# Kernel optimization log

Hardware: AMD Instinct MI355X
Metric: run time of the kernel (lower is better)

## Reference

```python
import jax, jax.numpy as jnp
import numpy as np

B, H, S, DK = 4, 16, 4096, 64


def setup_inputs() -> dict:
    key = jax.random.key(0)
    kq, kk, kv = jax.random.split(key, 3)
    Q = jax.random.normal(kq, (B, H, S, DK), dtype=jnp.float32)
    K = jax.random.normal(kk, (B, H, S, DK), dtype=jnp.float32)
    V = jax.random.normal(kv, (B, H, S, DK), dtype=jnp.float32)
    return {"Q": Q, "K": K, "V": V}


def reference(Q, K, V):
    d_k = K.shape[-1]
    inv_sqrt_dk = jnp.sqrt(jnp.float32(1.0) / d_k)
    # [B, H, S, S] materialized scores (faithful to the naive original)
    scores = jnp.einsum('bhqd,bhkd->bhqk', Q, K) * inv_sqrt_dk
    # causal mask: original subtracts (1 - tril) * 1e9 from scores
    s_q, s_k = Q.shape[-2], K.shape[-2]
    causal = jnp.tril(jnp.ones((s_q, s_k), dtype=jnp.float32))
    scores = scores - (1.0 - causal) * 1e9
    probs = jax.nn.softmax(scores, axis=-1)
    out = jnp.einsum('bhqk,bhkd->bhqd', probs, V)
    return out
```

## Files before the change

### kernel.cpp

```cpp
#include <hip/hip_runtime.h>
#include <hip/hip_bf16.h>

typedef short bf16x8 __attribute__((ext_vector_type(8)));
typedef float f32x16 __attribute__((ext_vector_type(16)));
typedef float f32x4v __attribute__((ext_vector_type(4)));

static constexpr int SEQ = 4096;
static constexpr int HD  = 64;
static constexpr int BQ  = 128;
static constexpr float QSCALE = 0.125f * 1.44269504088896340736f;

union F8 { bf16x8 v; unsigned short u[8]; uint4 q; };

__device__ __forceinline__ unsigned short f2bf(float x) {
    __bf16 b = (__bf16)x;
    return __builtin_bit_cast(unsigned short, b);
}
__device__ __forceinline__ unsigned pk2(float lo, float hi) {
    return (unsigned)f2bf(lo) | ((unsigned)f2bf(hi) << 16);
}
__device__ __forceinline__ float exp2fast(float x) {
    return __builtin_amdgcn_exp2f(x);
}

__device__ __forceinline__ int kperm_src(int rho) {
    return (rho & 0x23) | (((rho >> 3) & 1) << 4) |
           (((rho >> 2) & 1) << 3) | (((rho >> 4) & 1) << 2);
}
__device__ __forceinline__ int kperm_dst(int src) {
    return (src & 0x23) | (((src >> 2) & 1) << 4) |
           (((src >> 4) & 1) << 3) | (((src >> 3) & 1) << 2);
}

__global__ __launch_bounds__(256)
void prep_kv(const float* __restrict__ K, const float* __restrict__ V,
             unsigned short* __restrict__ ws)
{
    __shared__ float vt[64][68];

    const int tid = threadIdx.x;
    const int bid = blockIdx.x;
    const size_t sbase = ((size_t)(bid >> 6)) * (SEQ * HD) +
                         ((size_t)(bid & 63)) * (64 * HD);
    unsigned short* Kt = ws + (size_t)bid * 4096;
    unsigned short* Vt = ws + (size_t)16777216 + (size_t)bid * 4096;

    #pragma unroll
    for (int i = 0; i < 2; ++i) {
        const int c   = tid + 256 * i;
        const int row = c >> 3, j = c & 7;
        const int jsrc = j ^ (row & 7);
        const float* src = K + sbase + kperm_src(row) * HD + 8 * jsrc;
        float4 a = *(const float4*)src;
        float4 b = *(const float4*)(src + 4);
        *(uint4*)(Kt + row * 64 + 8 * j) =
            make_uint4(pk2(a.x, a.y), pk2(a.z, a.w), pk2(b.x, b.y), pk2(b.z, b.w));
    }

    {
        const int r  = tid >> 2;
        const int cb = (tid & 3) << 4;
        const float* src = V + sbase + r * HD + cb;
        *(float4*)&vt[r][cb + 0]  = *(const float4*)(src);
        *(float4*)&vt[r][cb + 4]  = *(const float4*)(src + 4);
        *(float4*)&vt[r][cb + 8]  = *(const float4*)(src + 8);
        *(float4*)&vt[r][cb + 12] = *(const float4*)(src + 12);
    }
    __syncthreads();
    #pragma unroll
    for (int i = 0; i < 2; ++i) {
        const int c = tid + 256 * i;
        const int d = c >> 3, j = c & 7;
        const int kb = 8 * (j ^ (d & 7));
        unsigned u[4];
        #pragma unroll
        for (int p = 0; p < 4; ++p)
            u[p] = pk2(vt[kb + 2 * p][d], vt[kb + 2 * p + 1][d]);
        *(uint4*)(Vt + d * 64 + 8 * j) = make_uint4(u[0], u[1], u[2], u[3]);
    }
}

__global__ __launch_bounds__(256, 2)
void mha_fwd2(const float* __restrict__ Q, float* __restrict__ O,
              const unsigned short* __restrict__ ws)
{
    __shared__ __align__(16) unsigned short LDSu[32768];

    const int tid  = threadIdx.x;
    const int lane = tid & 63;
    const int w    = tid >> 6;
    const int l31  = lane & 31;
    const int h    = lane >> 5;

    const int bid = blockIdx.x;
    const int bh  = bid & 63;
    const int qb  = 31 - (bid >> 6);
    const int q0  = qb * BQ;
    const size_t base = (size_t)bh * (SEQ * HD);

    const int qlane = q0 + 32 * w + l31;

    bf16x8 qf[4];
    {
        const float* qrow = Q + base + (size_t)qlane * HD;
        #pragma unroll
        for (int c = 0; c < 4; ++c) {
            const f32x4v x = *(const f32x4v*)(qrow + 16 * c + 8 * h);
            const f32x4v y = *(const f32x4v*)(qrow + 16 * c + 8 * h + 4);
            F8 f;
            #pragma unroll
            for (int j = 0; j < 4; ++j) f.u[j]     = f2bf(x[j] * QSCALE);
            #pragma unroll
            for (int j = 0; j < 4; ++j) f.u[4 + j] = f2bf(y[j] * QSCALE);
            qf[c] = f.v;
        }
    }

    F8 onesf;
    #pragma unroll
    for (int j = 0; j < 8; ++j) onesf.u[j] = 0x3F80;

    f32x16 oacc[2];
    f32x16 lacc;
    f32x16 zacc;
    #pragma unroll
    for (int r = 0; r < 16; ++r) {
        oacc[0][r] = 0.f; oacc[1][r] = 0.f; lacc[r] = 0.f; zacc[r] = 0.f;
    }

    const int nkt2 = qb + 1;

    char* lds0 = (char*)&LDSu[0];
    const int sw = (l31 & 7) << 4;
    char* a4[4];
    #pragma unroll
    for (int c = 0; c < 4; ++c)
        a4[c] = lds0 + l31 * 128 + (((c << 5) | (h << 4)) ^ sw);

    const unsigned short* Kws = ws;
    const unsigned short* Vws = ws + (size_t)16777216;

    auto stage = [&](int buf, int kt2) {
        const size_t toff = (((size_t)bh << 6) + ((size_t)kt2 << 1)) << 12;
        const int bufoff = buf << 14;
        #pragma unroll
        for (int i = 0; i < 4; ++i) {
            const int ch = 4 * w + i;
            const unsigned short* kg = Kws + toff + ch * 512 + lane * 8;
            const unsigned short* vg = Vws + toff + ch * 512 + lane * 8;
            __builtin_amdgcn_global_load_lds(
                (const __attribute__((address_space(1))) void*)(const void*)kg,
                (__attribute__((address_space(3))) void*)(void*)(lds0 + bufoff + ch * 1024),
                16, 0, 0);
            __builtin_amdgcn_global_load_lds(
                (const __attribute__((address_space(1))) void*)(const void*)vg,
                (__attribute__((address_space(3))) void*)(void*)(lds0 + 32768 + bufoff + ch * 1024),
                16, 0, 0);
        }
    };

    stage(0, 0);
    __syncthreads();

    for (int kt2 = 0; kt2 < nkt2; ++kt2) {
        const bool hn = (kt2 + 1) < nkt2;
        if (hn) stage((kt2 & 1) ^ 1, kt2 + 1);

        const int k0 = kt2 * 128;

        f32x16 sacc[4];
        #pragma unroll
        for (int s = 0; s < 4; ++s) {
            const int t = s >> 1, u = s & 1;
            __builtin_amdgcn_s_setprio(1);
            #pragma unroll
            for (int c = 0; c < 4; ++c) {
                bf16x8 kf = *(const bf16x8*)(a4[c] + t * 8192 + u * 4096);
                sacc[s] = __builtin_amdgcn_mfma_f32_32x32x16_bf16(
                    kf, qf[c], c == 0 ? zacc : sacc[s], 0, 0, 0);
            }
            __builtin_amdgcn_s_setprio(0);
        }

        if (kt2 == nkt2 - 1) {
            #pragma unroll
            for (int s = 0; s < 4; ++s)
                #pragma unroll
                for (int r = 0; r < 16; ++r) {
                    const int key = k0 + 64 * (s >> 1) + 32 * (s & 1) +
                                    16 * ((r >> 2) & 1) + 4 * ((r >> 3) & 1) +
                                    8 * h + (r & 3);
                    if (key > qlane) sacc[s][r] = -1e30f;
                }
        }

        #pragma unroll
        for (int kc = 0; kc < 8; ++kc) {
            const int s = kc >> 1, m0 = kc & 1;
            const int t = kc >> 2, kcl = kc & 3;
            float e0 = exp2fast(sacc[s][4 * m0 + 0]);
            float e1 = exp2fast(sacc[s][4 * m0 + 1]);
            float e2 = exp2fast(sacc[s][4 * m0 + 2]);
            float e3 = exp2fast(sacc[s][4 * m0 + 3]);
            float e4 = exp2fast(sacc[s][8 + 4 * m0 + 0]);
            float e5 = exp2fast(sacc[s][8 + 4 * m0 + 1]);
            float e6 = exp2fast(sacc[s][8 + 4 * m0 + 2]);
            float e7 = exp2fast(sacc[s][8 + 4 * m0 + 3]);
            F8 pf;
            pf.q.x = pk2(e0, e1);
            pf.q.y = pk2(e2, e3);
            pf.q.z = pk2(e4, e5);
            pf.q.w = pk2(e6, e7);
            __builtin_amdgcn_s_setprio(1);
            lacc = __builtin_amdgcn_mfma_f32_32x32x16_bf16(onesf.v, pf.v, lacc, 0, 0, 0);
            {
                bf16x8 vf0 = *(const bf16x8*)(a4[kcl] + 32768 + t * 8192 + 0 * 4096);
                oacc[0] = __builtin_amdgcn_mfma_f32_32x32x16_bf16(vf0, pf.v, oacc[0], 0, 0, 0);
                bf16x8 vf1 = *(const bf16x8*)(a4[kcl] + 32768 + t * 8192 + 1 * 4096);
                oacc[1] = __builtin_amdgcn_mfma_f32_32x32x16_bf16(vf1, pf.v, oacc[1], 0, 0, 0);
            }
            __builtin_amdgcn_s_setprio(0);
        }

        #pragma unroll
        for (int c = 0; c < 4; ++c)
            a4[c] = (char*)((size_t)a4[c] ^ 16384);

        __syncthreads();
    }

    const float il = 1.0f / lacc[0];
    float* orow = O + base + (size_t)qlane * HD;
    #pragma unroll
    for (int dsi = 0; dsi < 2; ++dsi)
        #pragma unroll
        for (int g = 0; g < 4; ++g) {
            f32x4v o4;
            #pragma unroll
            for (int j = 0; j < 4; ++j) o4[j] = oacc[dsi][4 * g + j] * il;
            *(f32x4v*)(orow + 32 * dsi + 8 * g + 4 * h) = o4;
        }
}

__global__ __launch_bounds__(256, 4)
void mha_fwd_fb(const float* __restrict__ Q, const float* __restrict__ K,
                const float* __restrict__ V, float* __restrict__ O)
{
    __shared__ unsigned short Kl[2][4096];
    __shared__ unsigned short Vl[2][4096];

    const int tid  = threadIdx.x;
    const int lane = tid & 63;
    const int w    = tid >> 6;
    const int l31  = lane & 31;
    const int h    = lane >> 5;

    const int bid = blockIdx.x;
    const int bh  = bid & 63;
    const int qb  = 31 - (bid >> 6);
    const int q0  = qb * BQ;
    const size_t base = (size_t)bh * (SEQ * HD);

    const int qlane  = q0 + 32 * w + l31;
    const int qmax_w = q0 + 32 * w + 31;

    bf16x8 qf[4];
    {
        const float* qrow = Q + base + (size_t)qlane * HD;
        #pragma unroll
        for (int c = 0; c < 4; ++c) {
            const f32x4v x = *(const f32x4v*)(qrow + 16 * c + 8 * h);
            const f32x4v y = *(const f32x4v*)(qrow + 16 * c + 8 * h + 4);
            F8 f;
            #pragma unroll
            for (int j = 0; j < 4; ++j) f.u[j]     = f2bf(x[j] * QSCALE);
            #pragma unroll
            for (int j = 0; j < 4; ++j) f.u[4 + j] = f2bf(y[j] * QSCALE);
            qf[c] = f.v;
        }
    }

    F8 onesf;
    #pragma unroll
    for (int j = 0; j < 8; ++j) onesf.u[j] = 0x3F80;

    f32x16 oacc[2], lacc, zacc;
    #pragma unroll
    for (int r = 0; r < 16; ++r) {
        oacc[0][r] = 0.f; oacc[1][r] = 0.f; lacc[r] = 0.f; zacc[r] = 0.f;
    }

    const int nkt = 2 * qb + 2;

    const int ksr = tid >> 2;
    const int ksc = (tid & 3) << 4;
    const int vkb = tid >> 4;
    const int vdb = tid & 15;

    f32x4v kreg[4], vreg[4];

    auto load_regs = [&](int kt) {
        const int k0 = kt * 64;
        const float* ks = K + base + (size_t)(k0 + ksr) * HD + ksc;
        kreg[0] = *(const f32x4v*)(ks);
        kreg[1] = *(const f32x4v*)(ks + 4);
        kreg[2] = *(const f32x4v*)(ks + 8);
        kreg[3] = *(const f32x4v*)(ks + 12);
        const float* vs = V + base + (size_t)(k0 + 4 * vkb) * HD + 4 * vdb;
        vreg[0] = *(const f32x4v*)(vs);
        vreg[1] = *(const f32x4v*)(vs + HD);
        vreg[2] = *(const f32x4v*)(vs + 2 * HD);
        vreg[3] = *(const f32x4v*)(vs + 3 * HD);
    };

    auto write_lds = [&](int buf) {
        unsigned u[8];
        #pragma unroll
        for (int i = 0; i < 4; ++i) {
            u[2*i]   = pk2(kreg[i][0], kreg[i][1]);
            u[2*i+1] = pk2(kreg[i][2], kreg[i][3]);
        }
        const int drow = kperm_dst(ksr);
        char* kd = (char*)&Kl[buf][0] + drow * 128;
        const int o0 = (2 * ksc) ^ ((drow & 7) << 4);
        *(uint4*)(kd + o0)        = make_uint4(u[0], u[1], u[2], u[3]);
        *(uint4*)(kd + (o0 ^ 16)) = make_uint4(u[4], u[5], u[6], u[7]);
        #pragma unroll
        for (int i = 0; i < 4; ++i) {
            const int c = (i + (vdb >> 1)) & 3;
            const int d = 4 * vdb + c;
            const unsigned lo = pk2(vreg[0][c], vreg[1][c]);
            const unsigned hi = pk2(vreg[2][c], vreg[3][c]);
            char* vd = (char*)&Vl[buf][0] + d * 128 + ((8 * vkb) ^ ((d & 7) << 4));
            *(uint2*)vd = make_uint2(lo, hi);
        }
    };

    load_regs(0); write_lds(0);
    __syncthreads();

    for (int kt = 0; kt < nkt; ++kt) {
        const int cur = kt & 1;
        const bool hn = (kt + 1) < nkt;
        if (hn) load_regs(kt + 1);

        if (64 * kt <= qmax_w) {
            const unsigned short* Kb = &Kl[cur][0];
            const unsigned short* Vb = &Vl[cur][0];
            const int k0 = kt * 64;

            f32x16 sacc[2];
            #pragma unroll
            for (int s = 0; s < 2; ++s) {
                const int row = 32 * s + l31;
                const char* rp = (const char*)Kb + row * 128;
                const int swl = (row & 7) << 4;
                #pragma unroll
                for (int c = 0; c < 4; ++c) {
                    bf16x8 kf = *(const bf16x8*)(rp + ((32 * c + 16 * h) ^ swl));
                    sacc[s] = __builtin_amdgcn_mfma_f32_32x32x16_bf16(
                        kf, qf[c], c == 0 ? zacc : sacc[s], 0, 0, 0);
                }
            }

            if (kt >= nkt - 2) {
                #pragma unroll
                for (int s = 0; s < 2; ++s)
                    #pragma unroll
                    for (int r = 0; r < 16; ++r) {
                        const int key = k0 + 32 * s + 16 * ((r >> 2) & 1) +
                                        4 * ((r >> 3) & 1) + 8 * h + (r & 3);
                        if (key > qlane) sacc[s][r] = -1e30f;
                    }
            }

            #pragma unroll
            for (int s = 0; s < 2; ++s) {
                #pragma unroll
                for (int r = 0; r < 16; ++r) sacc[s][r] = exp2fast(sacc[s][r]);
                #pragma unroll
                for (int m0 = 0; m0 < 2; ++m0) {
                    const int kc = 2 * s + m0;
                    F8 pf;
                    pf.q.x = pk2(sacc[s][4 * m0 + 0],  sacc[s][4 * m0 + 1]);
                    pf.q.y = pk2(sacc[s][4 * m0 + 2],  sacc[s][4 * m0 + 3]);
                    pf.q.z = pk2(sacc[s][8 + 4 * m0 + 0], sacc[s][8 + 4 * m0 + 1]);
                    pf.q.w = pk2(sacc[s][8 + 4 * m0 + 2], sacc[s][8 + 4 * m0 + 3]);
                    lacc = __builtin_amdgcn_mfma_f32_32x32x16_bf16(onesf.v, pf.v, lacc, 0, 0, 0);
                    #pragma unroll
                    for (int dsi = 0; dsi < 2; ++dsi) {
                        const int row = 32 * dsi + l31;
                        const char* vp = (const char*)Vb + row * 128 +
                                         ((32 * kc + 16 * h) ^ ((row & 7) << 4));
                        bf16x8 vf = *(const bf16x8*)vp;
                        oacc[dsi] = __builtin_amdgcn_mfma_f32_32x32x16_bf16(vf, pf.v, oacc[dsi], 0, 0, 0);
                    }
                }
            }
        }

        if (hn) write_lds(cur ^ 1);
        __syncthreads();
    }

    const float il = 1.0f / lacc[0];
    float* orow = O + base + (size_t)qlane * HD;
    #pragma unroll
    for (int dsi = 0; dsi < 2; ++dsi)
        #pragma unroll
        for (int g = 0; g < 4; ++g) {
            f32x4v o4;
            #pragma unroll
            for (int j = 0; j < 4; ++j) o4[j] = oacc[dsi][4 * g + j] * il;
            *(f32x4v*)(orow + 32 * dsi + 8 * g + 4 * h) = o4;
        }
}

extern "C" void kernel_launch(void* const* d_in, const int* in_sizes, int n_in,
                              void* d_out, int out_size, void* d_ws, size_t ws_size,
                              hipStream_t stream) {
    const float* Q = (const float*)d_in[0];
    const float* K = (const float*)d_in[1];
    const float* V = (const float*)d_in[2];
    float* O = (float*)d_out;
    (void)in_sizes; (void)n_in; (void)out_size;

    const size_t need = (size_t)2 * 16777216 * sizeof(unsigned short);
    if (ws_size >= need) {
        unsigned short* ws = (unsigned short*)d_ws;
        prep_kv<<<dim3(64 * 64), 256, 0, stream>>>(K, V, ws);
        mha_fwd2<<<dim3(32 * 64), 256, 0, stream>>>(Q, O, ws);
    } else {
        mha_fwd_fb<<<dim3(32 * 64), 256, 0, stream>>>(Q, K, V, O);
    }
}
```

Measured before the change: 255.5 us.

## Shrink KV tile to 64 keys with per-wave causal tile skipping

The attention kernel now steps through keys in 64-key tiles instead of 128, which halves LDS use so launch bounds rise to 4 blocks per CU. Each wave skips the compute for tiles that lie entirely above its own causal diagonal, and masking is applied only on the last two tiles. The aims are higher occupancy and less wasted work on masked keys, at the cost of twice as many loop iterations and block-wide barriers per KV range and possible register pressure at the higher occupancy target.

```diff
diff --git a/kernel.cpp b/kernel.cpp
--- a/kernel.cpp
+++ b/kernel.cpp
@@ -80,11 +80,11 @@
     }
 }
 
-__global__ __launch_bounds__(256, 2)
-void mha_fwd2(const float* __restrict__ Q, float* __restrict__ O,
-              const unsigned short* __restrict__ ws)
+__global__ __launch_bounds__(256, 4)
+void mha_fwd(const float* __restrict__ Q, float* __restrict__ O,
+             const unsigned short* __restrict__ ws)
 {
-    __shared__ __align__(16) unsigned short LDSu[32768];
+    __shared__ __align__(16) unsigned short LDSu[16384];
 
     const int tid  = threadIdx.x;
     const int lane = tid & 63;
@@ -98,7 +98,8 @@
     const int q0  = qb * BQ;
     const size_t base = (size_t)bh * (SEQ * HD);
 
-    const int qlane = q0 + 32 * w + l31;
+    const int qlane  = q0 + 32 * w + l31;
+    const int qmax_w = q0 + 32 * w + 31;
 
     bf16x8 qf[4];
     {
@@ -128,7 +129,7 @@
         oacc[0][r] = 0.f; oacc[1][r] = 0.f; lacc[r] = 0.f; zacc[r] = 0.f;
     }
 
-    const int nkt2 = qb + 1;
+    const int nkt = 2 * qb + 2;
 
     char* lds0 = (char*)&LDSu[0];
     const int sw = (l31 & 7) << 4;
@@ -140,12 +141,12 @@
     const unsigned short* Kws = ws;
     const unsigned short* Vws = ws + (size_t)16777216;
 
-    auto stage = [&](int buf, int kt2) {
-        const size_t toff = (((size_t)bh << 6) + ((size_t)kt2 << 1)) << 12;
-        const int bufoff = buf << 14;
-        #pragma unroll
-        for (int i = 0; i < 4; ++i) {
-            const int ch = 4 * w + i;
+    auto stage = [&](int buf, int kt) {
+        const size_t toff = (((size_t)bh << 6) + (size_t)kt) << 12;
+        const int bufoff = buf << 13;
+        #pragma unroll
+        for (int i = 0; i < 2; ++i) {
+            const int ch = 2 * w + i;
             const unsigned short* kg = Kws + toff + ch * 512 + lane * 8;
             const unsigned short* vg = Vws + toff + ch * 512 + lane * 8;
             __builtin_amdgcn_global_load_lds(
@@ -154,7 +155,7 @@
                 16, 0, 0);
             __builtin_amdgcn_global_load_lds(
                 (const __attribute__((address_space(1))) void*)(const void*)vg,
-                (__attribute__((address_space(3))) void*)(void*)(lds0 + 32768 + bufoff + ch * 1024),
+                (__attribute__((address_space(3))) void*)(void*)(lds0 + 16384 + bufoff + ch * 1024),
                 16, 0, 0);
         }
     };
@@ -162,69 +163,68 @@
     stage(0, 0);
     __syncthreads();
 
-    for (int kt2 = 0; kt2 < nkt2; ++kt2) {
-        const bool hn = (kt2 + 1) < nkt2;
-        if (hn) stage((kt2 & 1) ^ 1, kt2 + 1);
-
-        const int k0 = kt2 * 128;
-
-        f32x16 sacc[4];
-        #pragma unroll
-        for (int s = 0; s < 4; ++s) {
-            const int t = s >> 1, u = s & 1;
-            __builtin_amdgcn_s_setprio(1);
-            #pragma unroll
-            for (int c = 0; c < 4; ++c) {
-                bf16x8 kf = *(const bf16x8*)(a4[c] + t * 8192 + u * 4096);
-                sacc[s] = __builtin_amdgcn_mfma_f32_32x32x16_bf16(
-                    kf, qf[c], c == 0 ? zacc : sacc[s], 0, 0, 0);
-            }
-            __builtin_amdgcn_s_setprio(0);
-        }
-
-        if (kt2 == nkt2 - 1) {
-            #pragma unroll
-            for (int s = 0; s < 4; ++s)
-                #pragma unroll
-                for (int r = 0; r < 16; ++r) {
-                    const int key = k0 + 64 * (s >> 1) + 32 * (s & 1) +
-                                    16 * ((r >> 2) & 1) + 4 * ((r >> 3) & 1) +
-                                    8 * h + (r & 3);
-                    if (key > qlane) sacc[s][r] = -1e30f;
+    for (int kt = 0; kt < nkt; ++kt) {
+        const bool hn = (kt + 1) < nkt;
+        if (hn) stage((kt & 1) ^ 1, kt + 1);
+
+        if (64 * kt <= qmax_w) {
+            const int k0 = kt * 64;
+
+            f32x16 sacc[2];
+            #pragma unroll
+            for (int s = 0; s < 2; ++s) {
+                __builtin_amdgcn_s_setprio(1);
+                #pragma unroll
+                for (int c = 0; c < 4; ++c) {
+                    bf16x8 kf = *(const bf16x8*)(a4[c] + s * 4096);
+                    sacc[s] = __builtin_amdgcn_mfma_f32_32x32x16_bf16(
+                        kf, qf[c], c == 0 ? zacc : sacc[s], 0, 0, 0);
                 }
-        }
-
-        #pragma unroll
-        for (int kc = 0; kc < 8; ++kc) {
-            const int s = kc >> 1, m0 = kc & 1;
-            const int t = kc >> 2, kcl = kc & 3;
-            float e0 = exp2fast(sacc[s][4 * m0 + 0]);
-            float e1 = exp2fast(sacc[s][4 * m0 + 1]);
-            float e2 = exp2fast(sacc[s][4 * m0 + 2]);
-            float e3 = exp2fast(sacc[s][4 * m0 + 3]);
-            float e4 = exp2fast(sacc[s][8 + 4 * m0 + 0]);
-            float e5 = exp2fast(sacc[s][8 + 4 * m0 + 1]);
-            float e6 = exp2fast(sacc[s][8 + 4 * m0 + 2]);
-            float e7 = exp2fast(sacc[s][8 + 4 * m0 + 3]);
-            F8 pf;
-            pf.q.x = pk2(e0, e1);
-            pf.q.y = pk2(e2, e3);
-            pf.q.z = pk2(e4, e5);
-            pf.q.w = pk2(e6, e7);
-            __builtin_amdgcn_s_setprio(1);
-            lacc = __builtin_amdgcn_mfma_f32_32x32x16_bf16(onesf.v, pf.v, lacc, 0, 0, 0);
-            {
-                bf16x8 vf0 = *(const bf16x8*)(a4[kcl] + 32768 + t * 8192 + 0 * 4096);
-                oacc[0] = __builtin_amdgcn_mfma_f32_32x32x16_bf16(vf0, pf.v, oacc[0], 0, 0, 0);
-                bf16x8 vf1 = *(const bf16x8*)(a4[kcl] + 32768 + t * 8192 + 1 * 4096);
-                oacc[1] = __builtin_amdgcn_mfma_f32_32x32x16_bf16(vf1, pf.v, oacc[1], 0, 0, 0);
-            }
-            __builtin_amdgcn_s_setprio(0);
+                __builtin_amdgcn_s_setprio(0);
+            }
+
+            if (kt >= nkt - 2) {
+                #pragma unroll
+                for (int s = 0; s < 2; ++s)
+                    #pragma unroll
+                    for (int r = 0; r < 16; ++r) {
+                        const int key = k0 + 32 * s + 16 * ((r >> 2) & 1) +
+                                        4 * ((r >> 3) & 1) + 8 * h + (r & 3);
+                        if (key > qlane) sacc[s][r] = -1e30f;
+                    }
+            }
+
+            #pragma unroll
+            for (int kc = 0; kc < 4; ++kc) {
+                const int s = kc >> 1, m0 = kc & 1;
+                float e0 = exp2fast(sacc[s][4 * m0 + 0]);
+                float e1 = exp2fast(sacc[s][4 * m0 + 1]);
+                float e2 = exp2fast(sacc[s][4 * m0 + 2]);
+                float e3 = exp2fast(sacc[s][4 * m0 + 3]);
+                float e4 = exp2fast(sacc[s][8 + 4 * m0 + 0]);
+                float e5 = exp2fast(sacc[s][8 + 4 * m0 + 1]);
+                float e6 = exp2fast(sacc[s][8 + 4 * m0 + 2]);
+                float e7 = exp2fast(sacc[s][8 + 4 * m0 + 3]);
+                F8 pf;
+                pf.q.x = pk2(e0, e1);
+                pf.q.y = pk2(e2, e3);
+                pf.q.z = pk2(e4, e5);
+                pf.q.w = pk2(e6, e7);
+                __builtin_amdgcn_s_setprio(1);
+                lacc = __builtin_amdgcn_mfma_f32_32x32x16_bf16(onesf.v, pf.v, lacc, 0, 0, 0);
+                {
+                    bf16x8 vf0 = *(const bf16x8*)(a4[kc] + 16384 + 0 * 4096);
+                    oacc[0] = __builtin_amdgcn_mfma_f32_32x32x16_bf16(vf0, pf.v, oacc[0], 0, 0, 0);
+                    bf16x8 vf1 = *(const bf16x8*)(a4[kc] + 16384 + 1 * 4096);
+                    oacc[1] = __builtin_amdgcn_mfma_f32_32x32x16_bf16(vf1, pf.v, oacc[1], 0, 0, 0);
+                }
+                __builtin_amdgcn_s_setprio(0);
+            }
         }
 
         #pragma unroll
         for (int c = 0; c < 4; ++c)
-            a4[c] = (char*)((size_t)a4[c] ^ 16384);
+            a4[c] = (char*)((size_t)a4[c] ^ 8192);
 
         __syncthreads();
     }
@@ -429,7 +429,7 @@
     if (ws_size >= need) {
         unsigned short* ws = (unsigned short*)d_ws;
         prep_kv<<<dim3(64 * 64), 256, 0, stream>>>(K, V, ws);
-        mha_fwd2<<<dim3(32 * 64), 256, 0, stream>>>(Q, O, ws);
+        mha_fwd<<<dim3(32 * 64), 256, 0, stream>>>(Q, O, ws);
     } else {
         mha_fwd_fb<<<dim3(32 * 64), 256, 0, stream>>>(Q, K, V, O);
     }
```

After: 259.1 us. Within noise of the previous version (+1.4%).
